# Kernel optimization log

Hardware: AMD Instinct MI355X
Metric: run time of the kernel (lower is better)

The kernel has to match this reference:

```python
import jax, jax.numpy as jnp
import numpy as np

NR, NA = 2, 1                 # num_raw, num_angle
QDIM = NR + 2 * NA            # 4: [r, x1=cos(th), x2=sin(th)]
DQ = NR + NA                  # 3: [dr, dth]
D = 2 * NR + 3 * NA           # 7: full state dim
HID = 256
EPS = 1e-6


def setup_inputs() -> dict:
    key = jax.random.key(0)
    ks = jax.random.split(key, 4)
    B = 32768
    x = jax.random.normal(ks[0], (B, D), dtype=jnp.float32)
    W0 = jax.random.normal(ks[1], (HID, D), dtype=jnp.float32) / np.sqrt(D)
    b0 = jnp.zeros((HID,), dtype=jnp.float32)
    W1 = jax.random.normal(ks[2], (HID, HID), dtype=jnp.float32) / np.sqrt(HID)
    b1 = jnp.zeros((HID,), dtype=jnp.float32)
    W2 = jax.random.normal(ks[3], (1, HID), dtype=jnp.float32) / np.sqrt(HID)
    b2 = jnp.zeros((1,), dtype=jnp.float32)
    return {"x": x, "W0": W0, "b0": b0, "W1": W1, "b1": b1, "W2": W2, "b2": b2}


def _lnn_forward(x, W0, b0, W1, b1, W2, b2):
    def L_single(xi):  # scalar Lagrangian of one state (D,)
        h = jnp.tanh(W0 @ xi + b0)
        h = jnp.tanh(W1 @ h + b1)
        return (W2 @ h + b2)[0]

    grad_single = jax.grad(L_single)
    gradL = jax.vmap(grad_single)(x)                       # (B, D)

    # Rows of the Hessian corresponding to d/d(dr,dth): (B, DQ, D).
    # Replaces the torch per-row autograd.grad loop with one batched jacfwd.
    def g(xi):
        return grad_single(xi)[QDIM:]                      # dL/d(dr,dth), (DQ,)
    Hrows = jax.vmap(jax.jacfwd(g))(x)                     # (B, DQ, D)

    x1 = x[:, NR:NR + NA]                                  # cos part (B, NA)
    x2 = x[:, NR + NA:QDIM]                                # sin part (B, NA)

    Jr = Hrows[:, :, :NR]                                  # (B, DQ, NR)
    Jx1 = Hrows[:, :, NR:NR + NA]                          # (B, DQ, NA)
    Jx2 = Hrows[:, :, NR + NA:QDIM]                        # (B, DQ, NA)
    Hdq = Hrows[:, :, QDIM:] + EPS * jnp.eye(DQ, dtype=x.dtype)  # (B, DQ, DQ)

    # chain rule back to angle theta: d/dth = -x2 * d/dx1 + x1 * d/dx2
    Jth = -x2[:, None, :] * Jx1 + x1[:, None, :] * Jx2     # (B, DQ, NA)
    Jrth = jnp.concatenate([Jr, Jth], axis=2)              # (B, DQ, DQ)

    dLdr = gradL[:, :NR]
    dLdx1 = gradL[:, NR:NR + NA]
    dLdx2 = gradL[:, NR + NA:QDIM]
    dLdth = -x2 * dLdx1 + x1 * dLdx2
    dLdrdth = jnp.concatenate([dLdr, dLdth], axis=1)       # (B, DQ)

    dq = x[:, QDIM:]                                       # (B, DQ)
    dq_term = jnp.einsum('bij,bj->bi', Jrth, dq)

    rhs = dLdrdth - dq_term                                # control = 0 (no controlNet)
    ddq = jnp.linalg.solve(Hdq, rhs[..., None])[..., 0]    # (B, DQ)

    dr = dq[:, :NR]
    dth = dq[:, NR:]
    dx1 = -x2 * dth
    dx2 = x1 * dth
    return jnp.concatenate([dr, dx1, dx2, ddq], axis=1)    # (B, D)


def reference(x, W0, b0, W1, b1, W2, b2):
    return _lnn_forward(x, W0, b0, W1, b1, W2, b2)
```

## Files before the change

kernel.cpp:

```cpp
#include <hip/hip_runtime.h>
#include <math.h>

#define HID 256
#define EPS_REG 1e-6

typedef __attribute__((ext_vector_type(8))) short short8;
typedef __attribute__((ext_vector_type(4))) short short4v;
typedef __attribute__((ext_vector_type(4))) float v4f;

#define MFMA_BF16(a, b, c) __builtin_amdgcn_mfma_f32_16x16x32_bf16((a), (b), (c), 0, 0, 0)

__device__ __forceinline__ float fast_tanh(float z) {
    const float e = __expf(2.0f * z);
    const float d = e + 1.0f;
    float r = __builtin_amdgcn_rcpf(d);
    r = r * (2.0f - d * r);
    return fmaf(-2.0f, r, 1.0f);
}

__device__ __forceinline__ float rtn_bf16(float v, short* s) {
    unsigned r = (__float_as_uint(v) + 0x8000u) & 0xFFFF0000u;
    *s = (short)(r >> 16);
    return __uint_as_float(r);
}
__device__ __forceinline__ void split3(float v, short* a, short* b, short* c) {
    float f0 = rtn_bf16(v, a);
    float r1 = v - f0;
    float f1 = rtn_bf16(r1, b);
    float r2 = r1 - f1;
    (void)rtn_bf16(r2, c);
}

__global__ void prep_w1_frags(const float* __restrict__ W1, short* __restrict__ ws) {
    const int gid   = blockIdx.x * 128 + threadIdx.x;
    const int lane  = gid & 63;
    const int ks    = (gid >> 6) & 7;
    const int rt    = (gid >> 9) & 15;
    const int which = gid >> 13;
    const int m = lane & 15, q = lane >> 4;

    float v[8];
    if (which == 0) {
        const float* p = W1 + (size_t)(rt*16 + m)*HID + ks*32 + q*8;
        const float4 va = *(const float4*)(p);
        const float4 vb = *(const float4*)(p + 4);
        v[0]=va.x; v[1]=va.y; v[2]=va.z; v[3]=va.w;
        v[4]=vb.x; v[5]=vb.y; v[6]=vb.z; v[7]=vb.w;
    } else {
        const float* p = W1 + (size_t)(ks*32 + q*8)*HID + rt*16 + m;
#pragma unroll
        for (int t = 0; t < 8; ++t) v[t] = p[(size_t)t*HID];
    }
    short8 h8, m8, l8;
#pragma unroll
    for (int t = 0; t < 8; ++t) {
        short sh, sm, sl;
        split3(v[t], &sh, &sm, &sl);
        h8[t] = sh; m8[t] = sm; l8[t] = sl;
    }
    const size_t base = (size_t)which*3*65536 + ((size_t)(rt*8 + ks)*64 + lane)*8;
    *(short8*)(ws + base)          = h8;
    *(short8*)(ws + base + 65536)  = m8;
    *(short8*)(ws + base + 131072) = l8;
}

#define FRAG_NT_STRIDE 13056
#define FRAG_BUF_STRIDE 4352

__global__ __launch_bounds__(512, 4)
void lnn_mfma(const float* __restrict__ x,
              const float* __restrict__ W0, const float* __restrict__ b0,
              const float* __restrict__ b1, const float* __restrict__ W2,
              const short* __restrict__ ws,
              float* __restrict__ out)
{
    __shared__ __align__(16) short Bfrag[26112];
    __shared__ float M0h[HID * 9];

    const int tid   = threadIdx.x;
    const int samp0 = blockIdx.x * 8;
    const int lane  = tid & 63;
    const int w     = tid >> 6;

    {
        const int j  = tid & 255;
        const int s0 = (tid >> 8) * 4;
        float w0r[7];
#pragma unroll
        for (int d = 0; d < 7; ++d) w0r[d] = W0[j*7 + d];
        const float bj = b0[j];
        const int kbase = (j >> 3)*136 + (j & 7);
#pragma unroll
        for (int si = 0; si < 4; ++si) {
            const int s = s0 + si;
            const float* xs = x + (size_t)(samp0 + s)*7;
            float z = bj;
#pragma unroll
            for (int d = 0; d < 7; ++d) z = fmaf(w0r[d], xs[d], z);
            const float h  = fast_tanh(z);
            const float sg = 1.0f - h*h;
            M0h[j*9 + s] = h;
            const int nt = s >> 2;
            const int cb = (s & 3) * 4;
            float vals[4] = {h, sg*w0r[4], sg*w0r[5], sg*w0r[6]};
#pragma unroll
            for (int comp = 0; comp < 4; ++comp) {
                short sh, sm, sl;
                split3(vals[comp], &sh, &sm, &sl);
                const int a = nt*FRAG_NT_STRIDE + kbase + (cb + comp)*8;
                Bfrag[a]                    = sh;
                Bfrag[a + FRAG_BUF_STRIDE]  = sm;
                Bfrag[a + 2*FRAG_BUF_STRIDE]= sl;
            }
        }
    }
    __syncthreads();

    const short8* A1h = (const short8*)ws;
    const short8* A1m = A1h + 8192;
    const short8* A1l = A1h + 16384;
    const short8* A2h = A1h + 24576;
    const short8* A2m = A1h + 32768;
    const short8* A2l = A1h + 40960;

    const int q = lane >> 4;
    const int c = lane & 15;
    const int boff = q*136 + c*8;

    v4f acc[2][2];
#pragma unroll
    for (int rtl = 0; rtl < 2; ++rtl)
#pragma unroll
        for (int nt = 0; nt < 2; ++nt) acc[rtl][nt] = (v4f){0.f, 0.f, 0.f, 0.f};

    {
        short8 pah[2][2], pam[2][2], pal[2][2];
#pragma unroll
        for (int rtl = 0; rtl < 2; ++rtl) {
            const size_t fi = ((size_t)((w*2 + rtl)*8))*64 + lane;
            pah[0][rtl] = A1h[fi]; pam[0][rtl] = A1m[fi]; pal[0][rtl] = A1l[fi];
        }
#pragma unroll
        for (int ks = 0; ks < 8; ++ks) {
            const int cur = ks & 1, nxt = cur ^ 1;
            if (ks < 7) {
#pragma unroll
                for (int rtl = 0; rtl < 2; ++rtl) {
                    const size_t fi = ((size_t)((w*2 + rtl)*8 + ks + 1))*64 + lane;
                    pah[nxt][rtl] = A1h[fi]; pam[nxt][rtl] = A1m[fi]; pal[nxt][rtl] = A1l[fi];
                }
            }
            short8 bh[2], bm[2], bl[2];
#pragma unroll
            for (int nt = 0; nt < 2; ++nt) {
                const int a = nt*FRAG_NT_STRIDE + ks*544 + boff;
                bh[nt] = *(const short8*)(&Bfrag[a]);
                bm[nt] = *(const short8*)(&Bfrag[a + FRAG_BUF_STRIDE]);
                bl[nt] = *(const short8*)(&Bfrag[a + 2*FRAG_BUF_STRIDE]);
            }
#pragma unroll
            for (int rtl = 0; rtl < 2; ++rtl) {
                const short8 ah = pah[cur][rtl];
                const short8 am = pam[cur][rtl];
                const short8 al = pal[cur][rtl];
#pragma unroll
                for (int nt = 0; nt < 2; ++nt) {
                    acc[rtl][nt] = MFMA_BF16(ah, bl[nt], acc[rtl][nt]);
                    acc[rtl][nt] = MFMA_BF16(al, bh[nt], acc[rtl][nt]);
                    acc[rtl][nt] = MFMA_BF16(am, bm[nt], acc[rtl][nt]);
                    acc[rtl][nt] = MFMA_BF16(am, bh[nt], acc[rtl][nt]);
                    acc[rtl][nt] = MFMA_BF16(ah, bm[nt], acc[rtl][nt]);
                    acc[rtl][nt] = MFMA_BF16(ah, bh[nt], acc[rtl][nt]);
                }
            }
        }
    }
    __syncthreads();

    {
        const int myreg = c & 3;
#pragma unroll
        for (int rtl = 0; rtl < 2; ++rtl) {
            const int base = (w*2 + rtl)*16;
            float b1r[4], w2r[4];
#pragma unroll
            for (int r = 0; r < 4; ++r) {
                b1r[r] = b1[base + q*4 + r];
                w2r[r] = W2[base + q*4 + r];
            }
            const int G  = (base >> 3) + (q >> 1);
            const int tq = (q & 1) * 4;
#pragma unroll
            for (int nt = 0; nt < 2; ++nt) {
                short4v ph, pm, pl;
#pragma unroll
                for (int r = 0; r < 4; ++r) {
                    const float z0 = __shfl(acc[rtl][nt][r] + b1r[r], lane & ~3, 64);
                    const float h1 = fast_tanh(z0);
                    const float s1 = 1.0f - h1*h1;
                    const float av = acc[rtl][nt][r];
                    const float u  = (myreg == 0) ? (w2r[r]*s1)
                                                  : (-2.0f*w2r[r]*h1*s1)*av;
                    short sh, sm, sl;
                    split3(u, &sh, &sm, &sl);
                    ph[r] = sh; pm[r] = sm; pl[r] = sl;
                }
                const int a = nt*FRAG_NT_STRIDE + G*136 + c*8 + tq;
                *(short4v*)(&Bfrag[a])                     = ph;
                *(short4v*)(&Bfrag[a + FRAG_BUF_STRIDE])   = pm;
                *(short4v*)(&Bfrag[a + 2*FRAG_BUF_STRIDE]) = pl;
            }
        }
    }
    __syncthreads();

    v4f acc2[2][2];
#pragma unroll
    for (int rtl = 0; rtl < 2; ++rtl)
#pragma unroll
        for (int nt = 0; nt < 2; ++nt) acc2[rtl][nt] = (v4f){0.f, 0.f, 0.f, 0.f};

    {
        short8 pah[2][2], pam[2][2], pal[2][2];
#pragma unroll
        for (int rtl = 0; rtl < 2; ++rtl) {
            const size_t fi = ((size_t)((w*2 + rtl)*8))*64 + lane;
            pah[0][rtl] = A2h[fi]; pam[0][rtl] = A2m[fi]; pal[0][rtl] = A2l[fi];
        }
#pragma unroll
        for (int ks = 0; ks < 8; ++ks) {
            const int cur = ks & 1, nxt = cur ^ 1;
            if (ks < 7) {
#pragma unroll
                for (int rtl = 0; rtl < 2; ++rtl) {
                    const size_t fi = ((size_t)((w*2 + rtl)*8 + ks + 1))*64 + lane;
                    pah[nxt][rtl] = A2h[fi]; pam[nxt][rtl] = A2m[fi]; pal[nxt][rtl] = A2l[fi];
                }
            }
            short8 bh[2], bm[2], bl[2];
#pragma unroll
            for (int nt = 0; nt < 2; ++nt) {
                const int a = nt*FRAG_NT_STRIDE + ks*544 + boff;
                bh[nt] = *(const short8*)(&Bfrag[a]);
                bm[nt] = *(const short8*)(&Bfrag[a + FRAG_BUF_STRIDE]);
                bl[nt] = *(const short8*)(&Bfrag[a + 2*FRAG_BUF_STRIDE]);
            }
#pragma unroll
            for (int rtl = 0; rtl < 2; ++rtl) {
                const short8 ah = pah[cur][rtl];
                const short8 am = pam[cur][rtl];
                const short8 al = pal[cur][rtl];
#pragma unroll
                for (int nt = 0; nt < 2; ++nt) {
                    acc2[rtl][nt] = MFMA_BF16(ah, bl[nt], acc2[rtl][nt]);
                    acc2[rtl][nt] = MFMA_BF16(al, bh[nt], acc2[rtl][nt]);
                    acc2[rtl][nt] = MFMA_BF16(am, bm[nt], acc2[rtl][nt]);
                    acc2[rtl][nt] = MFMA_BF16(am, bh[nt], acc2[rtl][nt]);
                    acc2[rtl][nt] = MFMA_BF16(ah, bm[nt], acc2[rtl][nt]);
                    acc2[rtl][nt] = MFMA_BF16(ah, bh[nt], acc2[rtl][nt]);
                }
            }
        }
    }
    __syncthreads();

    {
        float* U0 = (float*)Bfrag;
#pragma unroll
        for (int rtl = 0; rtl < 2; ++rtl) {
#pragma unroll
            for (int reg = 0; reg < 4; ++reg) {
                const int j = (w*2 + rtl)*16 + q*4 + reg;
                const float w0sel = W0[j*7 + 3 + (c & 3)];
#pragma unroll
                for (int nt = 0; nt < 2; ++nt) {
                    const int s = nt*4 + (c >> 2);
                    const float pv = acc2[rtl][nt][reg];
                    const float p0 = __shfl(pv, lane & ~3, 64);
                    const float h0 = M0h[j*9 + s];
                    const float sg = 1.0f - h0*h0;
                    const float t2 = -2.0f * p0 * h0 * sg;
                    const float res = ((c & 3) == 0) ? (p0*sg)
                                                     : fmaf(pv, sg, t2 * w0sel);
                    U0[j*36 + s*4 + (c & 3)] = res;
                }
            }
        }
    }
    __syncthreads();

    const float* U0 = (const float*)Bfrag;
    float* scratch = ((float*)Bfrag) + 9216 + w * 425;
    const int s = w;
    const int t = tid & 63;
    float part[25];
#pragma unroll
    for (int qq = 0; qq < 25; ++qq) part[qq] = 0.0f;

#pragma unroll
    for (int m = 0; m < 4; ++m) {
        const int j = t + 64*m;
        const float4 uv = *(const float4*)(&U0[j*36 + s*4]);
        float w0d[7];
#pragma unroll
        for (int d = 0; d < 7; ++d) w0d[d] = W0[j*7 + d];
#pragma unroll
        for (int d = 0; d < 4; ++d) part[d] = fmaf(uv.x, w0d[d], part[d]);
#pragma unroll
        for (int d = 0; d < 7; ++d) {
            part[4  + d] = fmaf(uv.y, w0d[d], part[4  + d]);
            part[11 + d] = fmaf(uv.z, w0d[d], part[11 + d]);
            part[18 + d] = fmaf(uv.w, w0d[d], part[18 + d]);
        }
    }
#pragma unroll
    for (int off = 1; off <= 2; off <<= 1)
#pragma unroll
        for (int qq = 0; qq < 25; ++qq)
            part[qq] += __shfl_xor(part[qq], off, 64);
    {
        const int quad = t >> 2;
        if ((t & 3) == 0) {
#pragma unroll
            for (int e = 0; e < 25; ++e)
                scratch[e*17 + quad] = part[e];
        }
    }
    if (t < 25) {
        float tot = 0.0f;
#pragma unroll
        for (int k = 0; k < 16; ++k) tot += scratch[t*17 + k];
        scratch[t*17 + 16] = tot;
    }

    if (t == 0) {
        double g[25];
#pragma unroll
        for (int e = 0; e < 25; ++e) g[e] = (double)scratch[e*17 + 16];

        const float* xs = x + (size_t)(samp0 + s)*7;
        const double x1 = xs[2], x2 = xs[3];
        const double dq0 = xs[4], dq1 = xs[5], dth = xs[6];

        double M[3][3], rhs[3];
#pragma unroll
        for (int i = 0; i < 3; ++i) {
            const double J0 = g[4 + i*7 + 0];
            const double J1 = g[4 + i*7 + 1];
            const double J2 = -x2*g[4 + i*7 + 2] + x1*g[4 + i*7 + 3];
            const double dL = (i == 0) ? g[0]
                            : (i == 1) ? g[1]
                            : (-x2*g[2] + x1*g[3]);
            M[i][0] = g[4 + i*7 + 4] + (i == 0 ? EPS_REG : 0.0);
            M[i][1] = g[4 + i*7 + 5] + (i == 1 ? EPS_REG : 0.0);
            M[i][2] = g[4 + i*7 + 6] + (i == 2 ? EPS_REG : 0.0);
            rhs[i]  = dL - (J0*dq0 + J1*dq1 + J2*dth);
        }
        const double c00 = M[1][1]*M[2][2] - M[1][2]*M[2][1];
        const double c01 = M[1][2]*M[2][0] - M[1][0]*M[2][2];
        const double c02 = M[1][0]*M[2][1] - M[1][1]*M[2][0];
        const double det = M[0][0]*c00 + M[0][1]*c01 + M[0][2]*c02;
        const double inv = 1.0 / det;
        const double c10 = M[0][2]*M[2][1] - M[0][1]*M[2][2];
        const double c11 = M[0][0]*M[2][2] - M[0][2]*M[2][0];
        const double c12 = M[0][1]*M[2][0] - M[0][0]*M[2][1];
        const double c20 = M[0][1]*M[1][2] - M[0][2]*M[1][1];
        const double c21 = M[0][2]*M[1][0] - M[0][0]*M[1][2];
        const double c22 = M[0][0]*M[1][1] - M[0][1]*M[1][0];
        const double sol0 = (c00*rhs[0] + c10*rhs[1] + c20*rhs[2]) * inv;
        const double sol1 = (c01*rhs[0] + c11*rhs[1] + c21*rhs[2]) * inv;
        const double sol2 = (c02*rhs[0] + c12*rhs[1] + c22*rhs[2]) * inv;

        float* o = out + (size_t)(samp0 + s)*7;
        o[0] = (float)dq0;
        o[1] = (float)dq1;
        o[2] = (float)(-x2*dth);
        o[3] = (float)( x1*dth);
        o[4] = (float)sol0;
        o[5] = (float)sol1;
        o[6] = (float)sol2;
    }
}

#define TS8 8
#define SCP 36

__global__ void transpose_w1(const float* __restrict__ W1, float* __restrict__ W1T) {
    __shared__ float tile[32][33];
    const int bx = blockIdx.x & 7;
    const int by = blockIdx.x >> 3;
    const int tx = threadIdx.x & 31;
    const int ty = threadIdx.x >> 5;
#pragma unroll
    for (int q = 0; q < 4; ++q)
        tile[ty + q*8][tx] = W1[(by*32 + ty + q*8)*HID + bx*32 + tx];
    __syncthreads();
#pragma unroll
    for (int q = 0; q < 4; ++q)
        W1T[(bx*32 + ty + q*8)*HID + by*32 + tx] = tile[tx][ty + q*8];
}

__global__ __launch_bounds__(256, 2)
void lnn_fused(const float* __restrict__ x,
               const float* __restrict__ W0, const float* __restrict__ b0,
               const float* __restrict__ W1, const float* __restrict__ b1,
               const float* __restrict__ W2,
               const float* __restrict__ W1T, const int useT,
               float* __restrict__ out)
{
    __shared__ float M0[HID * SCP];
    __shared__ float U [HID * SCP];
    const int tid   = threadIdx.x;
    const int samp0 = blockIdx.x * TS8;
    {
        const int j = tid;
        float w0r[7];
#pragma unroll
        for (int d = 0; d < 7; ++d) w0r[d] = W0[j*7 + d];
        const float bj = b0[j];
#pragma unroll
        for (int s = 0; s < TS8; ++s) {
            const float* xs = x + (size_t)(samp0 + s)*7;
            float z = bj;
#pragma unroll
            for (int d = 0; d < 7; ++d) z = fmaf(w0r[d], xs[d], z);
            const float h  = tanhf(z);
            const float sg = 1.0f - h*h;
            float4 v = {h, sg * w0r[4], sg * w0r[5], sg * w0r[6]};
            *(float4*)(&M0[j*SCP + s*4]) = v;
        }
    }
    __syncthreads();
    const int it = tid & 63;
    const int ct = tid >> 6;
    float acc[4][8];
#pragma unroll
    for (int r = 0; r < 4; ++r)
#pragma unroll
        for (int c = 0; c < 8; ++c) acc[r][c] = 0.0f;
    if (useT) {
#pragma unroll 4
        for (int j = 0; j < HID; ++j) {
            const float4 w4 = *(const float4*)(W1T + (size_t)j*HID + it*4);
            const float4 ma = *(const float4*)(&M0[j*SCP + ct*8]);
            const float4 mb = *(const float4*)(&M0[j*SCP + ct*8 + 4]);
            const float w[4] = {w4.x, w4.y, w4.z, w4.w};
            const float m[8] = {ma.x, ma.y, ma.z, ma.w, mb.x, mb.y, mb.z, mb.w};
#pragma unroll
            for (int r = 0; r < 4; ++r)
#pragma unroll
                for (int c = 0; c < 8; ++c)
                    acc[r][c] = fmaf(w[r], m[c], acc[r][c]);
        }
    } else {
#pragma unroll 2
        for (int j = 0; j < HID; ++j) {
            float w[4];
#pragma unroll
            for (int r = 0; r < 4; ++r) w[r] = W1[(size_t)(it*4 + r)*HID + j];
            const float4 ma = *(const float4*)(&M0[j*SCP + ct*8]);
            const float4 mb = *(const float4*)(&M0[j*SCP + ct*8 + 4]);
            const float m[8] = {ma.x, ma.y, ma.z, ma.w, mb.x, mb.y, mb.z, mb.w};
#pragma unroll
            for (int r = 0; r < 4; ++r)
#pragma unroll
                for (int c = 0; c < 8; ++c)
                    acc[r][c] = fmaf(w[r], m[c], acc[r][c]);
        }
    }
    {
#pragma unroll
        for (int r = 0; r < 4; ++r) {
            const int i = it*4 + r;
            const float b1i = b1[i];
            const float w2i = W2[i];
#pragma unroll
            for (int cs = 0; cs < 2; ++cs) {
                const float z1 = acc[r][cs*4+0] + b1i;
                const float h1 = tanhf(z1);
                const float s1 = 1.0f - h1*h1;
                float4 uv;
                uv.x = w2i * s1;
                const float m2 = -2.0f * w2i * h1 * s1;
                uv.y = m2 * acc[r][cs*4+1];
                uv.z = m2 * acc[r][cs*4+2];
                uv.w = m2 * acc[r][cs*4+3];
                *(float4*)(&U[i*SCP + ct*8 + cs*4]) = uv;
            }
        }
    }
    __syncthreads();
    float acc2[4][8];
#pragma unroll
    for (int r = 0; r < 4; ++r)
#pragma unroll
        for (int c = 0; c < 8; ++c) acc2[r][c] = 0.0f;
#pragma unroll 4
    for (int i = 0; i < HID; ++i) {
        const float4 w4 = *(const float4*)(W1 + (size_t)i*HID + it*4);
        const float4 ua = *(const float4*)(&U[i*SCP + ct*8]);
        const float4 ub = *(const float4*)(&U[i*SCP + ct*8 + 4]);
        const float w[4] = {w4.x, w4.y, w4.z, w4.w};
        const float m[8] = {ua.x, ua.y, ua.z, ua.w, ub.x, ub.y, ub.z, ub.w};
#pragma unroll
        for (int r = 0; r < 4; ++r)
#pragma unroll
            for (int c = 0; c < 8; ++c)
                acc2[r][c] = fmaf(w[r], m[c], acc2[r][c]);
    }
    __syncthreads();
    {
#pragma unroll
        for (int r = 0; r < 4; ++r) {
            const int j = it*4 + r;
#pragma unroll
            for (int cs = 0; cs < 2; ++cs) {
                const int scb = ct*8 + cs*4;
                const float4 mm = *(const float4*)(&M0[j*SCP + scb]);
                const float h0v = mm.x;
                const float sg  = 1.0f - h0v*h0v;
                const float p   = acc2[r][cs*4+0];
                const float t2  = -2.0f * p * h0v;
                float4 uv;
                uv.x = p * sg;
                uv.y = fmaf(acc2[r][cs*4+1], sg, t2 * mm.y);
                uv.z = fmaf(acc2[r][cs*4+2], sg, t2 * mm.z);
                uv.w = fmaf(acc2[r][cs*4+3], sg, t2 * mm.w);
                *(float4*)(&U[j*SCP + scb]) = uv;
            }
        }
    }
    __syncthreads();
    const int s = tid >> 5;
    const int t = tid & 31;
    float part[25];
#pragma unroll
    for (int qq = 0; qq < 25; ++qq) part[qq] = 0.0f;
#pragma unroll
    for (int m = 0; m < 8; ++m) {
        const int j = t + 32*m;
        const float4 uv = *(const float4*)(&U[j*SCP + s*4]);
        float w0d[7];
#pragma unroll
        for (int d = 0; d < 7; ++d) w0d[d] = W0[j*7 + d];
#pragma unroll
        for (int d = 0; d < 4; ++d) part[d] = fmaf(uv.x, w0d[d], part[d]);
#pragma unroll
        for (int d = 0; d < 7; ++d) {
            part[4  + d] = fmaf(uv.y, w0d[d], part[4  + d]);
            part[11 + d] = fmaf(uv.z, w0d[d], part[11 + d]);
            part[18 + d] = fmaf(uv.w, w0d[d], part[18 + d]);
        }
    }
#pragma unroll
    for (int off = 16; off >= 1; off >>= 1)
#pragma unroll
        for (int qq = 0; qq < 25; ++qq)
            part[qq] += __shfl_xor(part[qq], off, 64);
    if (t == 0) {
        const float* xs = x + (size_t)(samp0 + s)*7;
        const double x1 = xs[2], x2 = xs[3];
        const double dq0 = xs[4], dq1 = xs[5], dth = xs[6];
        double A[3][4];
#pragma unroll
        for (int i = 0; i < 3; ++i) {
            const double J0 = part[4 + i*7 + 0];
            const double J1 = part[4 + i*7 + 1];
            const double J2 = -x2*(double)part[4 + i*7 + 2] + x1*(double)part[4 + i*7 + 3];
            const double dL = (i == 0) ? (double)part[0]
                            : (i == 1) ? (double)part[1]
                            : (-x2*(double)part[2] + x1*(double)part[3]);
            A[i][0] = (double)part[4 + i*7 + 4] + (i == 0 ? EPS_REG : 0.0);
            A[i][1] = (double)part[4 + i*7 + 5] + (i == 1 ? EPS_REG : 0.0);
            A[i][2] = (double)part[4 + i*7 + 6] + (i == 2 ? EPS_REG : 0.0);
            A[i][3] = dL - (J0*dq0 + J1*dq1 + J2*dth);
        }
        for (int cc = 0; cc < 2; ++cc) {
            int piv = cc;
            double mx = fabs(A[cc][cc]);
            for (int rr = cc + 1; rr < 3; ++rr) {
                const double v = fabs(A[rr][cc]);
                if (v > mx) { mx = v; piv = rr; }
            }
            if (piv != cc) {
                for (int k2 = 0; k2 < 4; ++k2) {
                    const double tmp = A[cc][k2]; A[cc][k2] = A[piv][k2]; A[piv][k2] = tmp;
                }
            }
            const double inv = 1.0 / A[cc][cc];
            for (int rr = cc + 1; rr < 3; ++rr) {
                const double f = A[rr][cc] * inv;
                for (int k2 = cc + 1; k2 < 4; ++k2) A[rr][k2] -= f * A[cc][k2];
            }
        }
        const double sol2 = A[2][3] / A[2][2];
        const double sol1 = (A[1][3] - A[1][2]*sol2) / A[1][1];
        const double sol0 = (A[0][3] - A[0][1]*sol1 - A[0][2]*sol2) / A[0][0];
        float* o = out + (size_t)(samp0 + s)*7;
        o[0] = (float)dq0;
        o[1] = (float)dq1;
        o[2] = (float)(-x2*dth);
        o[3] = (float)( x1*dth);
        o[4] = (float)sol0;
        o[5] = (float)sol1;
        o[6] = (float)sol2;
    }
}

extern "C" void kernel_launch(void* const* d_in, const int* in_sizes, int n_in,
                              void* d_out, int out_size, void* d_ws, size_t ws_size,
                              hipStream_t stream) {
    const float* x  = (const float*)d_in[0];
    const float* W0 = (const float*)d_in[1];
    const float* b0 = (const float*)d_in[2];
    const float* W1 = (const float*)d_in[3];
    const float* b1 = (const float*)d_in[4];
    const float* W2 = (const float*)d_in[5];
    float* out = (float*)d_out;

    const int B = in_sizes[0] / 7;
    const size_t NEED = 6u * 65536u * sizeof(short);

    if (ws_size >= NEED && (B % 8) == 0) {
        short* ws = (short*)d_ws;
        prep_w1_frags<<<128, 128, 0, stream>>>(W1, ws);
        lnn_mfma<<<B / 8, 512, 0, stream>>>(x, W0, b0, b1, W2, ws, out);
    } else {
        const int useT = (ws_size >= (size_t)HID * HID * sizeof(float)) ? 1 : 0;
        float* W1T = (float*)d_ws;
        if (useT) transpose_w1<<<64, 256, 0, stream>>>(W1, W1T);
        lnn_fused<<<B / TS8, 256, 0, stream>>>(x, W0, b0, W1, b1, W2, W1T, useT, out);
    }
}
```

Measured before the change: 267.1 us.

## Process two 8-sample groups per block with interleaved phases for overlap

Adds a new kernel in which each block handles 16 samples as two independent 8-sample groups, each with its own LDS buffers. The phases of the two groups are staggered so that one group's MFMA matmul runs between the same barriers as the other group's elementwise prologue or epilogue, which is meant to hide the latency of the scalar and LDS work behind matrix ops. It needs 120 KB of dynamic LDS, set through hipFuncSetAttribute, and lowers the occupancy hint from 4 to 2 blocks per CU. The old kernel is kept as a fallback, with its phases refactored into shared inline helpers.

```diff
diff --git a/kernel.cpp b/kernel.cpp
--- a/kernel.cpp
+++ b/kernel.cpp
@@ -66,232 +66,164 @@
 
 #define FRAG_NT_STRIDE 13056
 #define FRAG_BUF_STRIDE 4352
-
-__global__ __launch_bounds__(512, 4)
-void lnn_mfma(const float* __restrict__ x,
-              const float* __restrict__ W0, const float* __restrict__ b0,
-              const float* __restrict__ b1, const float* __restrict__ W2,
-              const short* __restrict__ ws,
-              float* __restrict__ out)
+#define BFRAG_SHORTS 26112
+#define M0H_FLOATS 2304
+#define FUSED_LDS_BYTES 122880
+
+__device__ __forceinline__ void lnn_phase0(const float* __restrict__ x,
+    const float* __restrict__ W0, const float* __restrict__ b0,
+    int samp_base, short* __restrict__ Bf, float* __restrict__ M0, int tid)
 {
-    __shared__ __align__(16) short Bfrag[26112];
-    __shared__ float M0h[HID * 9];
-
-    const int tid   = threadIdx.x;
-    const int samp0 = blockIdx.x * 8;
-    const int lane  = tid & 63;
-    const int w     = tid >> 6;
-
-    {
-        const int j  = tid & 255;
-        const int s0 = (tid >> 8) * 4;
-        float w0r[7];
-#pragma unroll
-        for (int d = 0; d < 7; ++d) w0r[d] = W0[j*7 + d];
-        const float bj = b0[j];
-        const int kbase = (j >> 3)*136 + (j & 7);
-#pragma unroll
-        for (int si = 0; si < 4; ++si) {
-            const int s = s0 + si;
-            const float* xs = x + (size_t)(samp0 + s)*7;
-            float z = bj;
-#pragma unroll
-            for (int d = 0; d < 7; ++d) z = fmaf(w0r[d], xs[d], z);
-            const float h  = fast_tanh(z);
-            const float sg = 1.0f - h*h;
-            M0h[j*9 + s] = h;
-            const int nt = s >> 2;
-            const int cb = (s & 3) * 4;
-            float vals[4] = {h, sg*w0r[4], sg*w0r[5], sg*w0r[6]};
-#pragma unroll
-            for (int comp = 0; comp < 4; ++comp) {
+    const int j  = tid & 255;
+    const int s0 = (tid >> 8) * 4;
+    float w0r[7];
+#pragma unroll
+    for (int d = 0; d < 7; ++d) w0r[d] = W0[j*7 + d];
+    const float bj = b0[j];
+    const int kbase = (j >> 3)*136 + (j & 7);
+#pragma unroll
+    for (int si = 0; si < 4; ++si) {
+        const int s = s0 + si;
+        const float* xs = x + (size_t)(samp_base + s)*7;
+        float z = bj;
+#pragma unroll
+        for (int d = 0; d < 7; ++d) z = fmaf(w0r[d], xs[d], z);
+        const float h  = fast_tanh(z);
+        const float sg = 1.0f - h*h;
+        M0[j*9 + s] = h;
+        const int nt = s >> 2;
+        const int cb = (s & 3) * 4;
+        float vals[4] = {h, sg*w0r[4], sg*w0r[5], sg*w0r[6]};
+#pragma unroll
+        for (int comp = 0; comp < 4; ++comp) {
+            short sh, sm, sl;
+            split3(vals[comp], &sh, &sm, &sl);
+            const int a = nt*FRAG_NT_STRIDE + kbase + (cb + comp)*8;
+            Bf[a]                     = sh;
+            Bf[a + FRAG_BUF_STRIDE]   = sm;
+            Bf[a + 2*FRAG_BUF_STRIDE] = sl;
+        }
+    }
+}
+
+__device__ __forceinline__ void lnn_mm(const short8* __restrict__ Ah,
+    const short8* __restrict__ Am, const short8* __restrict__ Al,
+    const short* __restrict__ Bf, int w, int lane, int boff, v4f acc[2][2])
+{
+    short8 pah[2][2], pam[2][2], pal[2][2];
+#pragma unroll
+    for (int rtl = 0; rtl < 2; ++rtl) {
+        const size_t fi = ((size_t)((w*2 + rtl)*8))*64 + lane;
+        pah[0][rtl] = Ah[fi]; pam[0][rtl] = Am[fi]; pal[0][rtl] = Al[fi];
+    }
+#pragma unroll
+    for (int ks = 0; ks < 8; ++ks) {
+        const int cur = ks & 1, nxt = cur ^ 1;
+        if (ks < 7) {
+#pragma unroll
+            for (int rtl = 0; rtl < 2; ++rtl) {
+                const size_t fi = ((size_t)((w*2 + rtl)*8 + ks + 1))*64 + lane;
+                pah[nxt][rtl] = Ah[fi]; pam[nxt][rtl] = Am[fi]; pal[nxt][rtl] = Al[fi];
+            }
+        }
+        short8 bh[2], bm[2], bl[2];
+#pragma unroll
+        for (int nt = 0; nt < 2; ++nt) {
+            const int a = nt*FRAG_NT_STRIDE + ks*544 + boff;
+            bh[nt] = *(const short8*)(&Bf[a]);
+            bm[nt] = *(const short8*)(&Bf[a + FRAG_BUF_STRIDE]);
+            bl[nt] = *(const short8*)(&Bf[a + 2*FRAG_BUF_STRIDE]);
+        }
+#pragma unroll
+        for (int rtl = 0; rtl < 2; ++rtl) {
+            const short8 ah = pah[cur][rtl];
+            const short8 am = pam[cur][rtl];
+            const short8 al = pal[cur][rtl];
+#pragma unroll
+            for (int nt = 0; nt < 2; ++nt) {
+                acc[rtl][nt] = MFMA_BF16(ah, bl[nt], acc[rtl][nt]);
+                acc[rtl][nt] = MFMA_BF16(al, bh[nt], acc[rtl][nt]);
+                acc[rtl][nt] = MFMA_BF16(am, bm[nt], acc[rtl][nt]);
+                acc[rtl][nt] = MFMA_BF16(am, bh[nt], acc[rtl][nt]);
+                acc[rtl][nt] = MFMA_BF16(ah, bm[nt], acc[rtl][nt]);
+                acc[rtl][nt] = MFMA_BF16(ah, bh[nt], acc[rtl][nt]);
+            }
+        }
+    }
+}
+
+__device__ __forceinline__ void lnn_epi1(v4f acc[2][2], short* __restrict__ Bf,
+    const float* __restrict__ b1, const float* __restrict__ W2,
+    int w, int lane, int q, int c)
+{
+    const int myreg = c & 3;
+#pragma unroll
+    for (int rtl = 0; rtl < 2; ++rtl) {
+        const int base = (w*2 + rtl)*16;
+        float b1r[4], w2r[4];
+#pragma unroll
+        for (int r = 0; r < 4; ++r) {
+            b1r[r] = b1[base + q*4 + r];
+            w2r[r] = W2[base + q*4 + r];
+        }
+        const int G  = (base >> 3) + (q >> 1);
+        const int tq = (q & 1) * 4;
+#pragma unroll
+        for (int nt = 0; nt < 2; ++nt) {
+            short4v ph, pm, pl;
+#pragma unroll
+            for (int r = 0; r < 4; ++r) {
+                const float z0 = __shfl(acc[rtl][nt][r] + b1r[r], lane & ~3, 64);
+                const float h1 = fast_tanh(z0);
+                const float s1 = 1.0f - h1*h1;
+                const float av = acc[rtl][nt][r];
+                const float u  = (myreg == 0) ? (w2r[r]*s1)
+                                              : (-2.0f*w2r[r]*h1*s1)*av;
                 short sh, sm, sl;
-                split3(vals[comp], &sh, &sm, &sl);
-                const int a = nt*FRAG_NT_STRIDE + kbase + (cb + comp)*8;
-                Bfrag[a]                    = sh;
-                Bfrag[a + FRAG_BUF_STRIDE]  = sm;
-                Bfrag[a + 2*FRAG_BUF_STRIDE]= sl;
-            }
-        }
-    }
-    __syncthreads();
-
-    const short8* A1h = (const short8*)ws;
-    const short8* A1m = A1h + 8192;
-    const short8* A1l = A1h + 16384;
-    const short8* A2h = A1h + 24576;
-    const short8* A2m = A1h + 32768;
-    const short8* A2l = A1h + 40960;
-
-    const int q = lane >> 4;
-    const int c = lane & 15;
-    const int boff = q*136 + c*8;
-
-    v4f acc[2][2];
-#pragma unroll
-    for (int rtl = 0; rtl < 2; ++rtl)
-#pragma unroll
-        for (int nt = 0; nt < 2; ++nt) acc[rtl][nt] = (v4f){0.f, 0.f, 0.f, 0.f};
-
-    {
-        short8 pah[2][2], pam[2][2], pal[2][2];
-#pragma unroll
-        for (int rtl = 0; rtl < 2; ++rtl) {
-            const size_t fi = ((size_t)((w*2 + rtl)*8))*64 + lane;
-            pah[0][rtl] = A1h[fi]; pam[0][rtl] = A1m[fi]; pal[0][rtl] = A1l[fi];
-        }
-#pragma unroll
-        for (int ks = 0; ks < 8; ++ks) {
-            const int cur = ks & 1, nxt = cur ^ 1;
-            if (ks < 7) {
-#pragma unroll
-                for (int rtl = 0; rtl < 2; ++rtl) {
-                    const size_t fi = ((size_t)((w*2 + rtl)*8 + ks + 1))*64 + lane;
-                    pah[nxt][rtl] = A1h[fi]; pam[nxt][rtl] = A1m[fi]; pal[nxt][rtl] = A1l[fi];
-                }
-            }
-            short8 bh[2], bm[2], bl[2];
+                split3(u, &sh, &sm, &sl);
+                ph[r] = sh; pm[r] = sm; pl[r] = sl;
+            }
+            const int a = nt*FRAG_NT_STRIDE + G*136 + c*8 + tq;
+            *(short4v*)(&Bf[a])                     = ph;
+            *(short4v*)(&Bf[a + FRAG_BUF_STRIDE])   = pm;
+            *(short4v*)(&Bf[a + 2*FRAG_BUF_STRIDE]) = pl;
+        }
+    }
+}
+
+__device__ __forceinline__ void lnn_epi2(v4f acc2[2][2], short* __restrict__ Bf,
+    const float* __restrict__ M0, const float* __restrict__ W0,
+    int w, int lane, int q, int c)
+{
+    float* U0 = (float*)Bf;
+#pragma unroll
+    for (int rtl = 0; rtl < 2; ++rtl) {
+#pragma unroll
+        for (int reg = 0; reg < 4; ++reg) {
+            const int j = (w*2 + rtl)*16 + q*4 + reg;
+            const float w0sel = W0[j*7 + 3 + (c & 3)];
 #pragma unroll
             for (int nt = 0; nt < 2; ++nt) {
-                const int a = nt*FRAG_NT_STRIDE + ks*544 + boff;
-                bh[nt] = *(const short8*)(&Bfrag[a]);
-                bm[nt] = *(const short8*)(&Bfrag[a + FRAG_BUF_STRIDE]);
-                bl[nt] = *(const short8*)(&Bfrag[a + 2*FRAG_BUF_STRIDE]);
-            }
-#pragma unroll
-            for (int rtl = 0; rtl < 2; ++rtl) {
-                const short8 ah = pah[cur][rtl];
-                const short8 am = pam[cur][rtl];
-                const short8 al = pal[cur][rtl];
-#pragma unroll
-                for (int nt = 0; nt < 2; ++nt) {
-                    acc[rtl][nt] = MFMA_BF16(ah, bl[nt], acc[rtl][nt]);
-                    acc[rtl][nt] = MFMA_BF16(al, bh[nt], acc[rtl][nt]);
-                    acc[rtl][nt] = MFMA_BF16(am, bm[nt], acc[rtl][nt]);
-                    acc[rtl][nt] = MFMA_BF16(am, bh[nt], acc[rtl][nt]);
-                    acc[rtl][nt] = MFMA_BF16(ah, bm[nt], acc[rtl][nt]);
-                    acc[rtl][nt] = MFMA_BF16(ah, bh[nt], acc[rtl][nt]);
-                }
-            }
-        }
-    }
-    __syncthreads();
-
-    {
-        const int myreg = c & 3;
-#pragma unroll
-        for (int rtl = 0; rtl < 2; ++rtl) {
-            const int base = (w*2 + rtl)*16;
-            float b1r[4], w2r[4];
-#pragma unroll
-            for (int r = 0; r < 4; ++r) {
-                b1r[r] = b1[base + q*4 + r];
-                w2r[r] = W2[base + q*4 + r];
-            }
-            const int G  = (base >> 3) + (q >> 1);
-            const int tq = (q & 1) * 4;
-#pragma unroll
-            for (int nt = 0; nt < 2; ++nt) {
-                short4v ph, pm, pl;
-#pragma unroll
-                for (int r = 0; r < 4; ++r) {
-                    const float z0 = __shfl(acc[rtl][nt][r] + b1r[r], lane & ~3, 64);
-                    const float h1 = fast_tanh(z0);
-                    const float s1 = 1.0f - h1*h1;
-                    const float av = acc[rtl][nt][r];
-                    const float u  = (myreg == 0) ? (w2r[r]*s1)
-                                                  : (-2.0f*w2r[r]*h1*s1)*av;
-                    short sh, sm, sl;
-                    split3(u, &sh, &sm, &sl);
-                    ph[r] = sh; pm[r] = sm; pl[r] = sl;
-                }
-                const int a = nt*FRAG_NT_STRIDE + G*136 + c*8 + tq;
-                *(short4v*)(&Bfrag[a])                     = ph;
-                *(short4v*)(&Bfrag[a + FRAG_BUF_STRIDE])   = pm;
-                *(short4v*)(&Bfrag[a + 2*FRAG_BUF_STRIDE]) = pl;
-            }
-        }
-    }
-    __syncthreads();
-
-    v4f acc2[2][2];
-#pragma unroll
-    for (int rtl = 0; rtl < 2; ++rtl)
-#pragma unroll
-        for (int nt = 0; nt < 2; ++nt) acc2[rtl][nt] = (v4f){0.f, 0.f, 0.f, 0.f};
-
-    {
-        short8 pah[2][2], pam[2][2], pal[2][2];
-#pragma unroll
-        for (int rtl = 0; rtl < 2; ++rtl) {
-            const size_t fi = ((size_t)((w*2 + rtl)*8))*64 + lane;
-            pah[0][rtl] = A2h[fi]; pam[0][rtl] = A2m[fi]; pal[0][rtl] = A2l[fi];
-        }
-#pragma unroll
-        for (int ks = 0; ks < 8; ++ks) {
-            const int cur = ks & 1, nxt = cur ^ 1;
-            if (ks < 7) {
-#pragma unroll
-                for (int rtl = 0; rtl < 2; ++rtl) {
-                    const size_t fi = ((size_t)((w*2 + rtl)*8 + ks + 1))*64 + lane;
-                    pah[nxt][rtl] = A2h[fi]; pam[nxt][rtl] = A2m[fi]; pal[nxt][rtl] = A2l[fi];
-                }
-            }
-            short8 bh[2], bm[2], bl[2];
-#pragma unroll
-            for (int nt = 0; nt < 2; ++nt) {
-                const int a = nt*FRAG_NT_STRIDE + ks*544 + boff;
-                bh[nt] = *(const short8*)(&Bfrag[a]);
-                bm[nt] = *(const short8*)(&Bfrag[a + FRAG_BUF_STRIDE]);
-                bl[nt] = *(const short8*)(&Bfrag[a + 2*FRAG_BUF_STRIDE]);
-            }
-#pragma unroll
-            for (int rtl = 0; rtl < 2; ++rtl) {
-                const short8 ah = pah[cur][rtl];
-                const short8 am = pam[cur][rtl];
-                const short8 al = pal[cur][rtl];
-#pragma unroll
-                for (int nt = 0; nt < 2; ++nt) {
-                    acc2[rtl][nt] = MFMA_BF16(ah, bl[nt], acc2[rtl][nt]);
-                    acc2[rtl][nt] = MFMA_BF16(al, bh[nt], acc2[rtl][nt]);
-                    acc2[rtl][nt] = MFMA_BF16(am, bm[nt], acc2[rtl][nt]);
-                    acc2[rtl][nt] = MFMA_BF16(am, bh[nt], acc2[rtl][nt]);
-                    acc2[rtl][nt] = MFMA_BF16(ah, bm[nt], acc2[rtl][nt]);
-                    acc2[rtl][nt] = MFMA_BF16(ah, bh[nt], acc2[rtl][nt]);
-                }
-            }
-        }
-    }
-    __syncthreads();
-
-    {
-        float* U0 = (float*)Bfrag;
-#pragma unroll
-        for (int rtl = 0; rtl < 2; ++rtl) {
-#pragma unroll
-            for (int reg = 0; reg < 4; ++reg) {
-                const int j = (w*2 + rtl)*16 + q*4 + reg;
-                const float w0sel = W0[j*7 + 3 + (c & 3)];
-#pragma unroll
-                for (int nt = 0; nt < 2; ++nt) {
-                    const int s = nt*4 + (c >> 2);
-                    const float pv = acc2[rtl][nt][reg];
-                    const float p0 = __shfl(pv, lane & ~3, 64);
-                    const float h0 = M0h[j*9 + s];
-                    const float sg = 1.0f - h0*h0;
-                    const float t2 = -2.0f * p0 * h0 * sg;
-                    const float res = ((c & 3) == 0) ? (p0*sg)
-                                                     : fmaf(pv, sg, t2 * w0sel);
-                    U0[j*36 + s*4 + (c & 3)] = res;
-                }
-            }
-        }
-    }
-    __syncthreads();
-
-    const float* U0 = (const float*)Bfrag;
-    float* scratch = ((float*)Bfrag) + 9216 + w * 425;
-    const int s = w;
+                const int s = nt*4 + (c >> 2);
+                const float pv = acc2[rtl][nt][reg];
+                const float p0 = __shfl(pv, lane & ~3, 64);
+                const float h0 = M0[j*9 + s];
+                const float sg = 1.0f - h0*h0;
+                const float t2 = -2.0f * p0 * h0 * sg;
+                const float res = ((c & 3) == 0) ? (p0*sg)
+                                                 : fmaf(pv, sg, t2 * w0sel);
+                U0[j*36 + s*4 + (c & 3)] = res;
+            }
+        }
+    }
+}
+
+__device__ __forceinline__ void lnn_phase3(const float* __restrict__ x,
+    const float* __restrict__ W0, short* __restrict__ Bf,
+    int samp_base, float* __restrict__ out, int w, int tid)
+{
+    const float* U0 = (const float*)Bf;
+    float* scratch = ((float*)Bf) + 9216 + w * 425;
     const int t = tid & 63;
     float part[25];
 #pragma unroll
@@ -300,7 +232,7 @@
 #pragma unroll
     for (int m = 0; m < 4; ++m) {
         const int j = t + 64*m;
-        const float4 uv = *(const float4*)(&U0[j*36 + s*4]);
+        const float4 uv = *(const float4*)(&U0[j*36 + w*4]);
         float w0d[7];
 #pragma unroll
         for (int d = 0; d < 7; ++d) w0d[d] = W0[j*7 + d];
@@ -338,7 +270,7 @@
 #pragma unroll
         for (int e = 0; e < 25; ++e) g[e] = (double)scratch[e*17 + 16];
 
-        const float* xs = x + (size_t)(samp0 + s)*7;
+        const float* xs = x + (size_t)(samp_base + w)*7;
         const double x1 = xs[2], x2 = xs[3];
         const double dq0 = xs[4], dq1 = xs[5], dth = xs[6];
 
@@ -371,7 +303,7 @@
         const double sol1 = (c01*rhs[0] + c11*rhs[1] + c21*rhs[2]) * inv;
         const double sol2 = (c02*rhs[0] + c12*rhs[1] + c22*rhs[2]) * inv;
 
-        float* o = out + (size_t)(samp0 + s)*7;
+        float* o = out + (size_t)(samp_base + w)*7;
         o[0] = (float)dq0;
         o[1] = (float)dq1;
         o[2] = (float)(-x2*dth);
@@ -380,6 +312,135 @@
         o[5] = (float)sol1;
         o[6] = (float)sol2;
     }
+}
+
+__global__ __launch_bounds__(512, 2)
+void lnn_mfma16(const float* __restrict__ x,
+                const float* __restrict__ W0, const float* __restrict__ b0,
+                const float* __restrict__ b1, const float* __restrict__ W2,
+                const short* __restrict__ ws,
+                float* __restrict__ out)
+{
+    extern __shared__ __align__(16) short smem[];
+    short* BfA = smem;
+    short* BfB = smem + BFRAG_SHORTS;
+    float* M0A = (float*)(smem + 2*BFRAG_SHORTS);
+    float* M0B = M0A + M0H_FLOATS;
+
+    const int tid   = threadIdx.x;
+    const int lane  = tid & 63;
+    const int w     = tid >> 6;
+    const int sampA = blockIdx.x * 16;
+    const int sampB = sampA + 8;
+    const int q = lane >> 4;
+    const int c = lane & 15;
+    const int boff = q*136 + c*8;
+
+    const short8* A1h = (const short8*)ws;
+    const short8* A1m = A1h + 8192;
+    const short8* A1l = A1h + 16384;
+    const short8* A2h = A1h + 24576;
+    const short8* A2m = A1h + 32768;
+    const short8* A2l = A1h + 40960;
+
+    lnn_phase0(x, W0, b0, sampA, BfA, M0A, tid);
+    __syncthreads();
+
+    v4f accA[2][2];
+#pragma unroll
+    for (int r = 0; r < 2; ++r)
+#pragma unroll
+        for (int n = 0; n < 2; ++n) accA[r][n] = (v4f){0.f, 0.f, 0.f, 0.f};
+    lnn_mm(A1h, A1m, A1l, BfA, w, lane, boff, accA);
+    lnn_phase0(x, W0, b0, sampB, BfB, M0B, tid);
+    __syncthreads();
+
+    v4f accB[2][2];
+#pragma unroll
+    for (int r = 0; r < 2; ++r)
+#pragma unroll
+        for (int n = 0; n < 2; ++n) accB[r][n] = (v4f){0.f, 0.f, 0.f, 0.f};
+    lnn_mm(A1h, A1m, A1l, BfB, w, lane, boff, accB);
+    lnn_epi1(accA, BfA, b1, W2, w, lane, q, c);
+    __syncthreads();
+
+    v4f acc2A[2][2];
+#pragma unroll
+    for (int r = 0; r < 2; ++r)
+#pragma unroll
+        for (int n = 0; n < 2; ++n) acc2A[r][n] = (v4f){0.f, 0.f, 0.f, 0.f};
+    lnn_mm(A2h, A2m, A2l, BfA, w, lane, boff, acc2A);
+    lnn_epi1(accB, BfB, b1, W2, w, lane, q, c);
+    __syncthreads();
+
+    v4f acc2B[2][2];
+#pragma unroll
+    for (int r = 0; r < 2; ++r)
+#pragma unroll
+        for (int n = 0; n < 2; ++n) acc2B[r][n] = (v4f){0.f, 0.f, 0.f, 0.f};
+    lnn_mm(A2h, A2m, A2l, BfB, w, lane, boff, acc2B);
+    lnn_epi2(acc2A, BfA, M0A, W0, w, lane, q, c);
+    __syncthreads();
+
+    lnn_epi2(acc2B, BfB, M0B, W0, w, lane, q, c);
+    lnn_phase3(x, W0, BfA, sampA, out, w, tid);
+    __syncthreads();
+
+    lnn_phase3(x, W0, BfB, sampB, out, w, tid);
+}
+
+__global__ __launch_bounds__(512, 4)
+void lnn_mfma(const float* __restrict__ x,
+              const float* __restrict__ W0, const float* __restrict__ b0,
+              const float* __restrict__ b1, const float* __restrict__ W2,
+              const short* __restrict__ ws,
+              float* __restrict__ out)
+{
+    __shared__ __align__(16) short Bfrag[26112];
+    __shared__ float M0h[HID * 9];
+
+    const int tid   = threadIdx.x;
+    const int samp0 = blockIdx.x * 8;
+    const int lane  = tid & 63;
+    const int w     = tid >> 6;
+
+    lnn_phase0(x, W0, b0, samp0, Bfrag, M0h, tid);
+    __syncthreads();
+
+    const short8* A1h = (const short8*)ws;
+    const short8* A1m = A1h + 8192;
+    const short8* A1l = A1h + 16384;
+    const short8* A2h = A1h + 24576;
+    const short8* A2m = A1h + 32768;
+    const short8* A2l = A1h + 40960;
+
+    const int q = lane >> 4;
+    const int c = lane & 15;
+    const int boff = q*136 + c*8;
+
+    v4f acc[2][2];
+#pragma unroll
+    for (int r = 0; r < 2; ++r)
+#pragma unroll
+        for (int n = 0; n < 2; ++n) acc[r][n] = (v4f){0.f, 0.f, 0.f, 0.f};
+    lnn_mm(A1h, A1m, A1l, Bfrag, w, lane, boff, acc);
+    __syncthreads();
+
+    lnn_epi1(acc, Bfrag, b1, W2, w, lane, q, c);
+    __syncthreads();
+
+    v4f acc2[2][2];
+#pragma unroll
+    for (int r = 0; r < 2; ++r)
+#pragma unroll
+        for (int n = 0; n < 2; ++n) acc2[r][n] = (v4f){0.f, 0.f, 0.f, 0.f};
+    lnn_mm(A2h, A2m, A2l, Bfrag, w, lane, boff, acc2);
+    __syncthreads();
+
+    lnn_epi2(acc2, Bfrag, M0h, W0, w, lane, q, c);
+    __syncthreads();
+
+    lnn_phase3(x, W0, Bfrag, samp0, out, w, tid);
 }
 
 #define TS8 8
@@ -621,7 +682,17 @@
     const int B = in_sizes[0] / 7;
     const size_t NEED = 6u * 65536u * sizeof(short);
 
-    if (ws_size >= NEED && (B % 8) == 0) {
+    static const bool big_lds_ok = [] {
+        return hipFuncSetAttribute(reinterpret_cast<const void*>(lnn_mfma16),
+                                   hipFuncAttributeMaxDynamicSharedMemorySize,
+                                   FUSED_LDS_BYTES) == hipSuccess;
+    }();
+
+    if (ws_size >= NEED && (B % 16) == 0 && big_lds_ok) {
+        short* ws = (short*)d_ws;
+        prep_w1_frags<<<128, 128, 0, stream>>>(W1, ws);
+        lnn_mfma16<<<B / 16, 512, FUSED_LDS_BYTES, stream>>>(x, W0, b0, b1, W2, ws, out);
+    } else if (ws_size >= NEED && (B % 8) == 0) {
         short* ws = (short*)d_ws;
         prep_w1_frags<<<128, 128, 0, stream>>>(W1, ws);
         lnn_mfma<<<B / 8, 512, 0, stream>>>(x, W0, b0, b1, W2, ws, out);
```

After: 335.2 us. 25.5% more time.
